# Kernel tuning notes

Measured on AMD Instinct MI355X. Metric: run time of the kernel, lower is better.

## Reference

```python
import jax, jax.numpy as jnp
import numpy as np

N = 8192
IN_DIM = 256
HIDDEN = 128


def setup_inputs() -> dict:
    key = jax.random.key(0)
    k1, k2 = jax.random.split(key)
    X = jax.random.normal(k1, (N, IN_DIM), dtype=jnp.float32)
    # nn.Linear(in_dim, hidden, bias=False): weight [hidden, in_dim]
    W = jax.random.normal(k2, (HIDDEN, IN_DIM), dtype=jnp.float32) * (1.0 / np.sqrt(IN_DIM))
    return {"X": X, "W": W}


def reference(X, W):
    # Z = X @ W.T : [N, hidden]
    Z = jnp.einsum('ni,hi->nh', X, W)
    # Dense similarity graph: ReLU(Z Z^T), row-normalized
    A = jax.nn.relu(jnp.einsum('nh,mh->nm', Z, Z))  # [N, N]
    A = A / (A.sum(axis=-1, keepdims=True) + 1e-6)
    out = jnp.einsum('nm,mh->nh', A, Z)  # [N, hidden]
    return (out, A)
```

## Files before the change

### kernel.cpp

```cpp
#include <hip/hip_runtime.h>


#define NR 8192
#define KD 256
#define HD 128

typedef short v8s __attribute__((ext_vector_type(8)));
typedef float v4f __attribute__((ext_vector_type(4)));

static __device__ __forceinline__ ushort f2bf(float f) {
    union { float f; unsigned u; } c; c.f = f;
    unsigned u = c.u;
    u += 0x7fffu + ((u >> 16) & 1u);
    return (ushort)(u >> 16);
}
static __device__ __forceinline__ float bf2f(ushort b) {
    union { unsigned u; float f; } c; c.u = ((unsigned)b) << 16; return c.f;
}
static __device__ __forceinline__ unsigned pk2(float a, float b) {
    union { float f; unsigned u; } x, y; x.f = a; y.f = b;
    unsigned ua = x.u + 0x7fffu + ((x.u >> 16) & 1u);
    unsigned ub = y.u + 0x7fffu + ((y.u >> 16) & 1u);
    return (ua >> 16) | (ub & 0xffff0000u);
}

__global__ __launch_bounds__(256) void k_z(const float* __restrict__ X,
                                           const float* __restrict__ W,
                                           ushort* __restrict__ Zb,
                                           ushort* __restrict__ ZbT) {
    __shared__ ushort Xhi[32][264];
    __shared__ ushort Xlo[32][264];
    int tid = threadIdx.x, lane = tid & 63, wave = tid >> 6;
    int lm = lane & 15, lq = lane >> 4;
    int n0 = blockIdx.x * 32;
    int hbase = wave * 32;
    v8s Whi[2][8], Wlo[2][8];
#pragma unroll
    for (int hi = 0; hi < 2; ++hi) {
        const float* wp = W + (hbase + hi * 16 + lm) * KD + lq * 8;
#pragma unroll
        for (int ks = 0; ks < 8; ++ks) {
            float4 w0 = *(const float4*)(wp + ks * 32);
            float4 w1 = *(const float4*)(wp + ks * 32 + 4);
            float wv[8] = {w0.x, w0.y, w0.z, w0.w, w1.x, w1.y, w1.z, w1.w};
#pragma unroll
            for (int j = 0; j < 8; ++j) {
                ushort h = f2bf(wv[j]);
                Whi[hi][ks][j] = (short)h;
                Wlo[hi][ks][j] = (short)f2bf(wv[j] - bf2f(h));
            }
        }
    }
#pragma unroll
    for (int t = 0; t < 8; ++t) {
        int idx = tid + t * 256;
        int r = idx >> 6, c4 = (idx & 63) * 4;
        float4 x = *(const float4*)(X + (size_t)(n0 + r) * KD + c4);
        ushort h0 = f2bf(x.x), h1 = f2bf(x.y), h2 = f2bf(x.z), h3 = f2bf(x.w);
        unsigned a = ((unsigned)h0) | ((unsigned)h1 << 16);
        unsigned b = ((unsigned)h2) | ((unsigned)h3 << 16);
        unsigned c = ((unsigned)f2bf(x.x - bf2f(h0))) | ((unsigned)f2bf(x.y - bf2f(h1)) << 16);
        unsigned d = ((unsigned)f2bf(x.z - bf2f(h2))) | ((unsigned)f2bf(x.w - bf2f(h3)) << 16);
        *(uint2*)&Xhi[r][c4] = make_uint2(a, b);
        *(uint2*)&Xlo[r][c4] = make_uint2(c, d);
    }
    __syncthreads();
#pragma unroll
    for (int ni = 0; ni < 2; ++ni) {
        v8s Ah[8], Al[8];
#pragma unroll
        for (int ks = 0; ks < 8; ++ks) {
            Ah[ks] = *(const v8s*)&Xhi[ni * 16 + lm][ks * 32 + lq * 8];
            Al[ks] = *(const v8s*)&Xlo[ni * 16 + lm][ks * 32 + lq * 8];
        }
        v4f acc[2] = {{0.f, 0.f, 0.f, 0.f}, {0.f, 0.f, 0.f, 0.f}};
#pragma unroll
        for (int ks = 0; ks < 8; ++ks)
#pragma unroll
            for (int hi = 0; hi < 2; ++hi) {
                acc[hi] = __builtin_amdgcn_mfma_f32_16x16x32_bf16(Ah[ks], Whi[hi][ks], acc[hi], 0, 0, 0);
                acc[hi] = __builtin_amdgcn_mfma_f32_16x16x32_bf16(Ah[ks], Wlo[hi][ks], acc[hi], 0, 0, 0);
                acc[hi] = __builtin_amdgcn_mfma_f32_16x16x32_bf16(Al[ks], Whi[hi][ks], acc[hi], 0, 0, 0);
            }
#pragma unroll
        for (int hi = 0; hi < 2; ++hi) {
            int h = hbase + hi * 16 + lm;
            int nb = n0 + ni * 16 + lq * 4;
            ushort b0 = f2bf(acc[hi][0]), b1 = f2bf(acc[hi][1]);
            ushort b2 = f2bf(acc[hi][2]), b3 = f2bf(acc[hi][3]);
            Zb[(size_t)(nb + 0) * HD + h] = b0;
            Zb[(size_t)(nb + 1) * HD + h] = b1;
            Zb[(size_t)(nb + 2) * HD + h] = b2;
            Zb[(size_t)(nb + 3) * HD + h] = b3;
            *(uint2*)&ZbT[(size_t)h * NR + nb] =
                make_uint2(((unsigned)b0) | ((unsigned)b1 << 16), ((unsigned)b2) | ((unsigned)b3 << 16));
        }
    }
}

__global__ __launch_bounds__(256) void k_rowsum(const ushort* __restrict__ Zb,
                                                float* __restrict__ rowsum) {
    __shared__ ushort ZC[128][136];
    int tid = threadIdx.x, lane = tid & 63, wave = tid >> 6;
    int lm = lane & 15, lq = lane >> 4;
    int rb = blockIdx.x >> 4, cs = blockIdx.x & 15;
    int row0 = rb * 128, cstart = cs * 512;
    int wr2 = wave >> 1, wc2 = wave & 1;
    v8s Bfr[4][4];
#pragma unroll
    for (int ri = 0; ri < 4; ++ri)
#pragma unroll
        for (int ks = 0; ks < 4; ++ks)
            Bfr[ri][ks] =
                *(const v8s*)(Zb + (size_t)(row0 + wr2 * 64 + ri * 16 + lm) * HD + ks * 32 + lq * 8);
    float rs[4] = {0.f, 0.f, 0.f, 0.f};
    for (int it = 0; it < 4; ++it) {
        int c0 = cstart + it * 128;
        __syncthreads();
#pragma unroll
        for (int t = 0; t < 8; ++t) {
            int idx = tid + t * 256;
            int r = idx >> 4, c8 = (idx & 15) * 8;
            *(uint4*)&ZC[r][c8] = *(const uint4*)(Zb + (size_t)(c0 + r) * HD + c8);
        }
        __syncthreads();
#pragma unroll
        for (int ci = 0; ci < 4; ++ci) {
            v8s Af[4];
#pragma unroll
            for (int ks = 0; ks < 4; ++ks)
                Af[ks] = *(const v8s*)&ZC[wc2 * 64 + ci * 16 + lm][ks * 32 + lq * 8];
            v4f acc[4] = {{0.f,0.f,0.f,0.f},{0.f,0.f,0.f,0.f},{0.f,0.f,0.f,0.f},{0.f,0.f,0.f,0.f}};
#pragma unroll
            for (int ks = 0; ks < 4; ++ks)
#pragma unroll
                for (int ri = 0; ri < 4; ++ri)
                    acc[ri] = __builtin_amdgcn_mfma_f32_16x16x32_bf16(Af[ks], Bfr[ri][ks], acc[ri], 0, 0, 0);
#pragma unroll
            for (int ri = 0; ri < 4; ++ri)
                rs[ri] += fmaxf(acc[ri][0], 0.f) + fmaxf(acc[ri][1], 0.f) +
                          fmaxf(acc[ri][2], 0.f) + fmaxf(acc[ri][3], 0.f);
        }
    }
#pragma unroll
    for (int ri = 0; ri < 4; ++ri) {
        float v = rs[ri];
        v += __shfl_xor(v, 16, 64);
        v += __shfl_xor(v, 32, 64);
        if (lq == 0) atomicAdd(&rowsum[row0 + wr2 * 64 + ri * 16 + lm], v);
    }
}

__global__ __launch_bounds__(256) void k_main(const ushort* __restrict__ Zb,
                                              const ushort* __restrict__ ZbT,
                                              const float* __restrict__ rowsum,
                                              float* __restrict__ outp,
                                              float* __restrict__ Ap) {
    __shared__ ushort ZC[2][64][136];
    __shared__ ushort PT[2][64][72];
    int tid = threadIdx.x, lane = tid & 63, wave = tid >> 6;
    int lm = lane & 15, lq = lane >> 4;
    int rb = blockIdx.x >> 3, cs = blockIdx.x & 7;
    int row0 = rb * 64, colb = cs * 1024;
    int wr2 = wave >> 1, wc2 = wave & 1;
    v8s Bfr[2][4];
#pragma unroll
    for (int ri = 0; ri < 2; ++ri)
#pragma unroll
        for (int ks = 0; ks < 4; ++ks)
            Bfr[ri][ks] =
                *(const v8s*)(Zb + (size_t)(row0 + wr2 * 32 + ri * 16 + lm) * HD + ks * 32 + lq * 8);
    float rsv[2];
#pragma unroll
    for (int ri = 0; ri < 2; ++ri)
        rsv[ri] = 1.0f / (rowsum[row0 + wr2 * 32 + ri * 16 + lm] + 1e-6f);
    v4f U[2][4];
#pragma unroll
    for (int ri = 0; ri < 2; ++ri)
#pragma unroll
        for (int hi = 0; hi < 4; ++hi) U[ri][hi] = (v4f){0.f, 0.f, 0.f, 0.f};

#pragma unroll
    for (int t = 0; t < 4; ++t) {
        int idx = tid + t * 256;
        int r = idx >> 4, c8 = (idx & 15) * 8;
        *(uint4*)&ZC[0][r][c8] = *(const uint4*)(Zb + (size_t)(colb + r) * HD + c8);
    }
    __syncthreads();

    float* ap0 = Ap + (size_t)(row0 + wr2 * 32 + lm) * NR + colb + wc2 * 32 + lq * 4;
    float* ap1 = ap0 + (size_t)16 * NR;

    for (int it = 0; it < 16; ++it) {
        int cur = it & 1;
        int c0 = colb + it * 64;
        uint4 sr[4];
        if (it < 15) {
#pragma unroll
            for (int t = 0; t < 4; ++t) {
                int idx = tid + t * 256;
                int r = idx >> 4, c8 = (idx & 15) * 8;
                sr[t] = *(const uint4*)(Zb + (size_t)(c0 + 64 + r) * HD + c8);
            }
        }
        v8s Bz[4][2];
#pragma unroll
        for (int hi = 0; hi < 4; ++hi)
#pragma unroll
            for (int ks = 0; ks < 2; ++ks)
                Bz[hi][ks] = *(const v8s*)(ZbT + (size_t)(wc2 * 64 + hi * 16 + lm) * NR + c0 +
                                           ks * 32 + lq * 8);
        v4f avst[2][2];
#pragma unroll
        for (int ci = 0; ci < 2; ++ci) {
            v8s Af[4];
#pragma unroll
            for (int ks = 0; ks < 4; ++ks)
                Af[ks] = *(const v8s*)&ZC[cur][wc2 * 32 + ci * 16 + lm][ks * 32 + lq * 8];
            v4f S0 = {0.f, 0.f, 0.f, 0.f}, S1 = {0.f, 0.f, 0.f, 0.f};
#pragma unroll
            for (int ks = 0; ks < 4; ++ks) {
                S0 = __builtin_amdgcn_mfma_f32_16x16x32_bf16(Af[ks], Bfr[0][ks], S0, 0, 0, 0);
                S1 = __builtin_amdgcn_mfma_f32_16x16x32_bf16(Af[ks], Bfr[1][ks], S1, 0, 0, 0);
            }
            int cb = wc2 * 32 + ci * 16 + lq * 4;
            {
                v4f av;
                av[0] = fmaxf(S0[0], 0.f) * rsv[0]; av[1] = fmaxf(S0[1], 0.f) * rsv[0];
                av[2] = fmaxf(S0[2], 0.f) * rsv[0]; av[3] = fmaxf(S0[3], 0.f) * rsv[0];
                avst[ci][0] = av;
                *(uint2*)&PT[cur][wr2 * 32 + lm][cb] = make_uint2(pk2(av[0], av[1]), pk2(av[2], av[3]));
            }
            {
                v4f av;
                av[0] = fmaxf(S1[0], 0.f) * rsv[1]; av[1] = fmaxf(S1[1], 0.f) * rsv[1];
                av[2] = fmaxf(S1[2], 0.f) * rsv[1]; av[3] = fmaxf(S1[3], 0.f) * rsv[1];
                avst[ci][1] = av;
                *(uint2*)&PT[cur][wr2 * 32 + 16 + lm][cb] =
                    make_uint2(pk2(av[0], av[1]), pk2(av[2], av[3]));
            }
        }
        if (it < 15) {
#pragma unroll
            for (int t = 0; t < 4; ++t) {
                int idx = tid + t * 256;
                int r = idx >> 4, c8 = (idx & 15) * 8;
                *(uint4*)&ZC[cur ^ 1][r][c8] = sr[t];
            }
        }
        __syncthreads();
#pragma unroll
        for (int ci = 0; ci < 2; ++ci) {
            __builtin_nontemporal_store(avst[ci][0], (v4f*)(ap0 + ci * 16));
            __builtin_nontemporal_store(avst[ci][1], (v4f*)(ap1 + ci * 16));
        }
#pragma unroll
        for (int ks = 0; ks < 2; ++ks) {
            v8s P0 = *(const v8s*)&PT[cur][wr2 * 32 + lm][ks * 32 + lq * 8];
            v8s P1 = *(const v8s*)&PT[cur][wr2 * 32 + 16 + lm][ks * 32 + lq * 8];
#pragma unroll
            for (int hi = 0; hi < 4; ++hi) {
                U[0][hi] = __builtin_amdgcn_mfma_f32_16x16x32_bf16(P0, Bz[hi][ks], U[0][hi], 0, 0, 0);
                U[1][hi] = __builtin_amdgcn_mfma_f32_16x16x32_bf16(P1, Bz[hi][ks], U[1][hi], 0, 0, 0);
            }
        }
        ap0 += 64;
        ap1 += 64;
    }
#pragma unroll
    for (int ri = 0; ri < 2; ++ri)
#pragma unroll
        for (int hi = 0; hi < 4; ++hi)
#pragma unroll
            for (int j = 0; j < 4; ++j)
                atomicAdd(&outp[(size_t)(row0 + wr2 * 32 + ri * 16 + lq * 4 + j) * HD +
                                wc2 * 64 + hi * 16 + lm],
                          U[ri][hi][j]);
}

extern "C" void kernel_launch(void* const* d_in, const int* in_sizes, int n_in,
                              void* d_out, int out_size, void* d_ws, size_t ws_size,
                              hipStream_t stream) {
    (void)in_sizes; (void)n_in; (void)out_size; (void)ws_size;
    const float* X = (const float*)d_in[0];
    const float* W = (const float*)d_in[1];
    float* outp = (float*)d_out;
    float* Ap = outp + (size_t)NR * HD;
    char* ws = (char*)d_ws;
    ushort* Zb = (ushort*)ws;
    ushort* ZbT = (ushort*)(ws + (size_t)NR * HD * 2);
    float* rowsum = (float*)(ws + (size_t)NR * HD * 4);

    (void)hipMemsetAsync(outp, 0, (size_t)NR * HD * sizeof(float), stream);
    (void)hipMemsetAsync(rowsum, 0, NR * sizeof(float), stream);
    k_z<<<dim3(NR / 32), dim3(256), 0, stream>>>(X, W, Zb, ZbT);
    k_rowsum<<<dim3(1024), dim3(256), 0, stream>>>(Zb, rowsum);
    k_main<<<dim3(1024), dim3(256), 0, stream>>>(Zb, ZbT, rowsum, outp, Ap);
}
```

Baseline: 370.1 us.

## Double-buffer rowsum column tiles and halve Z-projection block size

```diff
diff --git a/kernel.cpp b/kernel.cpp
--- a/kernel.cpp
+++ b/kernel.cpp
@@ -28,11 +28,11 @@
                                            const float* __restrict__ W,
                                            ushort* __restrict__ Zb,
                                            ushort* __restrict__ ZbT) {
-    __shared__ ushort Xhi[32][264];
-    __shared__ ushort Xlo[32][264];
+    __shared__ ushort Xhi[16][264];
+    __shared__ ushort Xlo[16][264];
     int tid = threadIdx.x, lane = tid & 63, wave = tid >> 6;
     int lm = lane & 15, lq = lane >> 4;
-    int n0 = blockIdx.x * 32;
+    int n0 = blockIdx.x * 16;
     int hbase = wave * 32;
     v8s Whi[2][8], Wlo[2][8];
 #pragma unroll
@@ -52,7 +52,7 @@
         }
     }
 #pragma unroll
-    for (int t = 0; t < 8; ++t) {
+    for (int t = 0; t < 4; ++t) {
         int idx = tid + t * 256;
         int r = idx >> 6, c4 = (idx & 63) * 4;
         float4 x = *(const float4*)(X + (size_t)(n0 + r) * KD + c4);
@@ -65,13 +65,12 @@
         *(uint2*)&Xlo[r][c4] = make_uint2(c, d);
     }
     __syncthreads();
-#pragma unroll
-    for (int ni = 0; ni < 2; ++ni) {
+    {
         v8s Ah[8], Al[8];
 #pragma unroll
         for (int ks = 0; ks < 8; ++ks) {
-            Ah[ks] = *(const v8s*)&Xhi[ni * 16 + lm][ks * 32 + lq * 8];
-            Al[ks] = *(const v8s*)&Xlo[ni * 16 + lm][ks * 32 + lq * 8];
+            Ah[ks] = *(const v8s*)&Xhi[lm][ks * 32 + lq * 8];
+            Al[ks] = *(const v8s*)&Xlo[lm][ks * 32 + lq * 8];
         }
         v4f acc[2] = {{0.f, 0.f, 0.f, 0.f}, {0.f, 0.f, 0.f, 0.f}};
 #pragma unroll
@@ -85,7 +84,7 @@
 #pragma unroll
         for (int hi = 0; hi < 2; ++hi) {
             int h = hbase + hi * 16 + lm;
-            int nb = n0 + ni * 16 + lq * 4;
+            int nb = n0 + lq * 4;
             ushort b0 = f2bf(acc[hi][0]), b1 = f2bf(acc[hi][1]);
             ushort b2 = f2bf(acc[hi][2]), b3 = f2bf(acc[hi][3]);
             Zb[(size_t)(nb + 0) * HD + h] = b0;
@@ -100,54 +99,69 @@
 
 __global__ __launch_bounds__(256) void k_rowsum(const ushort* __restrict__ Zb,
                                                 float* __restrict__ rowsum) {
-    __shared__ ushort ZC[128][136];
+    __shared__ ushort ZC[2][64][136];
     int tid = threadIdx.x, lane = tid & 63, wave = tid >> 6;
     int lm = lane & 15, lq = lane >> 4;
     int rb = blockIdx.x >> 4, cs = blockIdx.x & 15;
     int row0 = rb * 128, cstart = cs * 512;
-    int wr2 = wave >> 1, wc2 = wave & 1;
-    v8s Bfr[4][4];
-#pragma unroll
-    for (int ri = 0; ri < 4; ++ri)
+    v8s Bfr[2][4];
+#pragma unroll
+    for (int ri = 0; ri < 2; ++ri)
 #pragma unroll
         for (int ks = 0; ks < 4; ++ks)
             Bfr[ri][ks] =
-                *(const v8s*)(Zb + (size_t)(row0 + wr2 * 64 + ri * 16 + lm) * HD + ks * 32 + lq * 8);
-    float rs[4] = {0.f, 0.f, 0.f, 0.f};
-    for (int it = 0; it < 4; ++it) {
-        int c0 = cstart + it * 128;
-        __syncthreads();
-#pragma unroll
-        for (int t = 0; t < 8; ++t) {
-            int idx = tid + t * 256;
-            int r = idx >> 4, c8 = (idx & 15) * 8;
-            *(uint4*)&ZC[r][c8] = *(const uint4*)(Zb + (size_t)(c0 + r) * HD + c8);
-        }
-        __syncthreads();
+                *(const v8s*)(Zb + (size_t)(row0 + wave * 32 + ri * 16 + lm) * HD + ks * 32 + lq * 8);
+    float rs[2] = {0.f, 0.f};
+#pragma unroll
+    for (int t = 0; t < 4; ++t) {
+        int idx = tid + t * 256;
+        int r = idx >> 4, c8 = (idx & 15) * 8;
+        *(uint4*)&ZC[0][r][c8] = *(const uint4*)(Zb + (size_t)(cstart + r) * HD + c8);
+    }
+    __syncthreads();
+    for (int it = 0; it < 8; ++it) {
+        int cur = it & 1;
+        int c0 = cstart + it * 64;
+        uint4 sr[4];
+        if (it < 7) {
+#pragma unroll
+            for (int t = 0; t < 4; ++t) {
+                int idx = tid + t * 256;
+                int r = idx >> 4, c8 = (idx & 15) * 8;
+                sr[t] = *(const uint4*)(Zb + (size_t)(c0 + 64 + r) * HD + c8);
+            }
+        }
 #pragma unroll
         for (int ci = 0; ci < 4; ++ci) {
             v8s Af[4];
 #pragma unroll
             for (int ks = 0; ks < 4; ++ks)
-                Af[ks] = *(const v8s*)&ZC[wc2 * 64 + ci * 16 + lm][ks * 32 + lq * 8];
-            v4f acc[4] = {{0.f,0.f,0.f,0.f},{0.f,0.f,0.f,0.f},{0.f,0.f,0.f,0.f},{0.f,0.f,0.f,0.f}};
-#pragma unroll
-            for (int ks = 0; ks < 4; ++ks)
-#pragma unroll
-                for (int ri = 0; ri < 4; ++ri)
-                    acc[ri] = __builtin_amdgcn_mfma_f32_16x16x32_bf16(Af[ks], Bfr[ri][ks], acc[ri], 0, 0, 0);
-#pragma unroll
-            for (int ri = 0; ri < 4; ++ri)
-                rs[ri] += fmaxf(acc[ri][0], 0.f) + fmaxf(acc[ri][1], 0.f) +
-                          fmaxf(acc[ri][2], 0.f) + fmaxf(acc[ri][3], 0.f);
-        }
-    }
-#pragma unroll
-    for (int ri = 0; ri < 4; ++ri) {
+                Af[ks] = *(const v8s*)&ZC[cur][ci * 16 + lm][ks * 32 + lq * 8];
+            v4f a0 = {0.f, 0.f, 0.f, 0.f}, a1 = {0.f, 0.f, 0.f, 0.f};
+#pragma unroll
+            for (int ks = 0; ks < 4; ++ks) {
+                a0 = __builtin_amdgcn_mfma_f32_16x16x32_bf16(Af[ks], Bfr[0][ks], a0, 0, 0, 0);
+                a1 = __builtin_amdgcn_mfma_f32_16x16x32_bf16(Af[ks], Bfr[1][ks], a1, 0, 0, 0);
+            }
+            rs[0] += fmaxf(a0[0], 0.f) + fmaxf(a0[1], 0.f) + fmaxf(a0[2], 0.f) + fmaxf(a0[3], 0.f);
+            rs[1] += fmaxf(a1[0], 0.f) + fmaxf(a1[1], 0.f) + fmaxf(a1[2], 0.f) + fmaxf(a1[3], 0.f);
+        }
+        if (it < 7) {
+#pragma unroll
+            for (int t = 0; t < 4; ++t) {
+                int idx = tid + t * 256;
+                int r = idx >> 4, c8 = (idx & 15) * 8;
+                *(uint4*)&ZC[cur ^ 1][r][c8] = sr[t];
+            }
+        }
+        __syncthreads();
+    }
+#pragma unroll
+    for (int ri = 0; ri < 2; ++ri) {
         float v = rs[ri];
         v += __shfl_xor(v, 16, 64);
         v += __shfl_xor(v, 32, 64);
-        if (lq == 0) atomicAdd(&rowsum[row0 + wr2 * 64 + ri * 16 + lm], v);
+        if (lq == 0) atomicAdd(&rowsum[row0 + wave * 32 + ri * 16 + lm], v);
     }
 }
 
@@ -293,7 +307,7 @@
 
     (void)hipMemsetAsync(outp, 0, (size_t)NR * HD * sizeof(float), stream);
     (void)hipMemsetAsync(rowsum, 0, NR * sizeof(float), stream);
-    k_z<<<dim3(NR / 32), dim3(256), 0, stream>>>(X, W, Zb, ZbT);
+    k_z<<<dim3(NR / 16), dim3(256), 0, stream>>>(X, W, Zb, ZbT);
     k_rowsum<<<dim3(1024), dim3(256), 0, stream>>>(Zb, rowsum);
     k_main<<<dim3(1024), dim3(256), 0, stream>>>(Zb, ZbT, rowsum, outp, Ap);
 }
```

Result: faster. 361.9 us (-2.2%).
